# Optimization experiments

Measured on AMD Instinct MI355X. Metric: run time of the kernel, lower is better.

## Reference

```python
import math
import jax, jax.numpy as jnp
import numpy as np

H = 512        # d_model
NST = 32       # N // 2 complex states
M = 2          # frac_M
CH = 1         # channels
L_DEFAULT = 2048
OMIN, OMAX = 1e-06, 100.0
EMIN, EMAX = 1e-06, 10.0


def _logit_init(vals, vmin, vmax):
    v = np.clip(np.asarray(vals, np.float32), vmin, vmax)
    p = np.clip((v - vmin) / (vmax - vmin), 1e-06, 1.0 - 1e-06)
    return np.log(p / (1.0 - p)).astype(np.float32)


def setup_inputs() -> dict:
    key = jax.random.key(0)
    k1, k2 = jax.random.split(key, 2)
    # log_dt ~ U[log(dt_min), log(dt_max)]
    log_dt = (jax.random.uniform(k1, (H,), dtype=jnp.float32)
              * (math.log(0.1) - math.log(0.001)) + math.log(0.001))
    # C stored as real view of complex [CH, H, NST]
    C_real = jax.random.normal(k2, (CH, H, NST, 2), dtype=jnp.float32)
    log_A_real = jnp.log(0.5 * jnp.ones((H, NST), jnp.float32))
    A_imag = math.pi * jnp.broadcast_to(jnp.arange(NST, dtype=jnp.float32), (H, NST))
    # frac_M == 2 defaults: omega=[0.0, 0.1], eta=[1.0, 0.1], stored as logits
    omega_logit = jnp.asarray(_logit_init([0.0, 0.1], OMIN, OMAX))
    eta_logit = jnp.asarray(_logit_init([1.0, 0.1], EMIN, EMAX))
    return {"C_real": C_real, "log_dt": log_dt, "log_A_real": log_A_real,
            "A_imag": A_imag, "omega_logit": omega_logit,
            "eta_logit": eta_logit, "L": L_DEFAULT}


def reference(C_real, log_dt, log_A_real, A_imag, omega_logit, eta_logit, L):
    dt = jnp.exp(log_dt)                                   # [H]
    C = C_real[..., 0] + 1j * C_real[..., 1]               # [CH, H, NST] complex
    A = -jnp.exp(log_A_real) + 1j * A_imag                 # [H, NST] complex
    omega = OMIN + jax.nn.sigmoid(omega_logit) * (OMAX - OMIN)  # [M]
    eta = EMIN + jax.nn.sigmoid(eta_logit) * (EMAX - EMIN)      # [M]
    # fractional mixture of poles: A_frac[h, m, n] = -omega_m + eta_m * A[h, n]
    A_frac = (-omega[None, :, None] + eta[None, :, None] * A[:, None, :]).reshape(H, M * NST)
    C_frac = (eta[None, None, :, None] * C[:, :, None, :]).reshape(CH, H, M * NST)
    dtA = A_frac * dt[:, None]                             # [H, M*NST]
    exp_dtA = jnp.exp(dtA)
    small = jnp.abs(A_frac) < 1e-06
    C_disc = C_frac * (exp_dtA[None] - 1.0) / (A_frac[None] + 1e-08)
    C_disc = jnp.where(small[None], C_frac * dt[None, :, None], C_disc)
    t = jnp.arange(L, dtype=jnp.float32)
    exp_K = jnp.exp(dtA[:, :, None] * t)                   # [H, M*NST, L] complex Vandermonde
    K = 2.0 * jnp.einsum('chn,hnl->chl', C_disc, exp_K).real  # [CH, H, L]
    return K
```

## Files before the change

kernel.cpp:

```cpp
#include <hip/hip_runtime.h>
#include <math.h>

#define HH   512
#define NST  32
#define MM   2
#define LL   2048
#define NS   (MM * NST)
#define TL   8

__global__ __launch_bounds__(256) void loong_kernel(
    const float* __restrict__ C_real,
    const float* __restrict__ log_dt,
    const float* __restrict__ log_A_real,
    const float* __restrict__ A_imag,
    const float* __restrict__ omega_logit,
    const float* __restrict__ eta_logit,
    float* __restrict__ out)
{
    __shared__ float4 sT1[NS][16];
    __shared__ float4 sT2[NS][16];

    const int h   = blockIdx.x;
    const int tid = threadIdx.x;

    if (tid < NS) {
        const int m = tid >> 5;
        const int n = tid & 31;
        const float dt  = expf(log_dt[h]);
        const float Are = -expf(log_A_real[h * NST + n]);
        const float Aim = A_imag[h * NST + n];
        const float om = 1e-6f + (100.0f - 1e-6f) / (1.0f + expf(-omega_logit[m]));
        const float et = 1e-6f + (10.0f  - 1e-6f) / (1.0f + expf(-eta_logit[m]));
        const float Afr = fmaf(et, Are, -om);
        const float Afi = et * Aim;
        const float Cfr = et * C_real[(h * NST + n) * 2 + 0];
        const float Cfi = et * C_real[(h * NST + n) * 2 + 1];
        const float ar = dt * Afr, ai = dt * Afi;
        const float e = expf(ar);
        float sn, cs;
        sincosf(ai, &sn, &cs);
        const float Er = e * cs, Ei = e * sn;
        const float dr = Afr + 1e-8f, di = Afi;
        const float inv = 1.0f / fmaf(dr, dr, di * di);
        const float numr = Er - 1.0f, numi = Ei;
        const float fr = fmaf(numr, dr,  numi * di) * inv;
        const float fi = fmaf(numi, dr, -numr * di) * inv;
        float Cdr = fmaf(Cfr, fr, -(Cfi * fi));
        float Cdi = fmaf(Cfr, fi,  (Cfi * fr));
        if (sqrtf(fmaf(Afr, Afr, Afi * Afi)) < 1e-6f) {
            Cdr = Cfr * dt;
            Cdi = Cfi * dt;
        }
        const float Ccr = 2.0f * Cdr, Cci = 2.0f * Cdi;
        const float p  = 2.0f * Er;
        const float qc = -fmaf(Er, Er, Ei * Ei);

        float w2r = fmaf(Er, Er, -(Ei * Ei)),  w2i = 2.0f * Er * Ei;
        float w4r = fmaf(w2r, w2r, -(w2i * w2i)), w4i = 2.0f * w2r * w2i;
        float w8r = fmaf(w4r, w4r, -(w4i * w4i)), w8i = 2.0f * w4r * w4i;

        float ur = 1.0f, ui = 0.0f;
#pragma unroll
        for (int r = 0; r < 16; ++r) {
            sT1[tid][r] = make_float4(ur, ui,
                                      fmaf(ur, Er, -(ui * Ei)),
                                      fmaf(ur, Ei,  (ui * Er)));
            const float nr = fmaf(ur, w8r, -(ui * w8i));
            const float ni = fmaf(ur, w8i,  (ui * w8r));
            ur = nr; ui = ni;
        }
        float wr_ = w8r, wi_ = w8i;
#pragma unroll
        for (int k = 0; k < 4; ++k) {
            const float nr = fmaf(wr_, wr_, -(wi_ * wi_));
            const float ni = 2.0f * wr_ * wi_;
            wr_ = nr; wi_ = ni;
        }
        float vr = Ccr, vi = Cci;
#pragma unroll
        for (int q = 0; q < 16; ++q) {
            sT2[tid][q] = make_float4(vr, vi, p, qc);
            const float nr = fmaf(vr, wr_, -(vi * wi_));
            const float ni = fmaf(vr, wi_,  (vi * wr_));
            vr = nr; vi = ni;
        }
    }
    __syncthreads();

    const int ri = tid & 15;
    const int qi = tid >> 4;

    float acc[TL];
#pragma unroll
    for (int j = 0; j < TL; ++j) acc[j] = 0.0f;

    for (int s = 0; s < NS; s += 4) {
        float4 t1[4], t2[4];
#pragma unroll
        for (int u = 0; u < 4; ++u) {
            t1[u] = sT1[s + u][ri];
            t2[u] = sT2[s + u][qi];
        }
#pragma unroll
        for (int u = 0; u < 4; ++u) {
            const float p = t2[u].z, qq = t2[u].w;
            float r0 = fmaf(t1[u].x, t2[u].x, -(t1[u].y * t2[u].y));
            float r1 = fmaf(t1[u].z, t2[u].x, -(t1[u].w * t2[u].y));
            acc[0] += r0;
            acc[1] += r1;
#pragma unroll
            for (int j = 2; j < TL; ++j) {
                const float rn = fmaf(p, r1, qq * r0);
                acc[j] += rn;
                r0 = r1; r1 = rn;
            }
        }
    }

    float4* o = reinterpret_cast<float4*>(out + (size_t)h * LL + (size_t)tid * TL);
    o[0] = make_float4(acc[0], acc[1], acc[2], acc[3]);
    o[1] = make_float4(acc[4], acc[5], acc[6], acc[7]);
}

extern "C" void kernel_launch(void* const* d_in, const int* in_sizes, int n_in,
                              void* d_out, int out_size, void* d_ws, size_t ws_size,
                              hipStream_t stream) {
    const float* C_real      = (const float*)d_in[0];
    const float* log_dt      = (const float*)d_in[1];
    const float* log_A_real  = (const float*)d_in[2];
    const float* A_imag      = (const float*)d_in[3];
    const float* omega_logit = (const float*)d_in[4];
    const float* eta_logit   = (const float*)d_in[5];
    float* out = (float*)d_out;

    loong_kernel<<<dim3(HH), dim3(256), 0, stream>>>(
        C_real, log_dt, log_A_real, A_imag, omega_logit, eta_logit, out);
}
```

Measured before the change: 74.92 us.

## Spread table setup over all threads, swizzle LDS tables, double-buffer LDS loads

Table setup now runs on all 256 threads: each of the 64 states is split into four parts, and each part writes 8 of the 16 T1 or T2 entries, seeded with w^64 or w^1024 jumps. Before, only 64 threads built the tables serially. The LDS tables are XOR-swizzled by state index to spread the accesses across shared-memory banks. The main loop is double-buffered so LDS reads for the next group of states are issued while the current group is computed. The trade is more redundant pole and exp computation per thread, and more registers for the two load buffers.

```diff
diff --git a/kernel.cpp b/kernel.cpp
--- a/kernel.cpp
+++ b/kernel.cpp
@@ -23,9 +23,11 @@
     const int h   = blockIdx.x;
     const int tid = threadIdx.x;
 
-    if (tid < NS) {
-        const int m = tid >> 5;
-        const int n = tid & 31;
+    {
+        const int s    = tid & (NS - 1);
+        const int part = tid >> 6;
+        const int m = s >> 5;
+        const int n = s & 31;
         const float dt  = expf(log_dt[h]);
         const float Are = -expf(log_A_real[h * NST + n]);
         const float Aim = A_imag[h * NST + n];
@@ -55,34 +57,47 @@
         const float p  = 2.0f * Er;
         const float qc = -fmaf(Er, Er, Ei * Ei);
 
-        float w2r = fmaf(Er, Er, -(Ei * Ei)),  w2i = 2.0f * Er * Ei;
-        float w4r = fmaf(w2r, w2r, -(w2i * w2i)), w4i = 2.0f * w2r * w2i;
-        float w8r = fmaf(w4r, w4r, -(w4i * w4i)), w8i = 2.0f * w4r * w4i;
+        const float w2r = fmaf(Er, Er, -(Ei * Ei)),     w2i = 2.0f * Er * Ei;
+        const float w4r = fmaf(w2r, w2r, -(w2i * w2i)), w4i = 2.0f * w2r * w2i;
+        const float w8r = fmaf(w4r, w4r, -(w4i * w4i)), w8i = 2.0f * w4r * w4i;
+        const float w16r  = fmaf(w8r,  w8r,  -(w8i  * w8i)),  w16i  = 2.0f * w8r  * w8i;
+        const float w32r  = fmaf(w16r, w16r, -(w16i * w16i)), w32i  = 2.0f * w16r * w16i;
+        const float w64r  = fmaf(w32r, w32r, -(w32i * w32i)), w64i  = 2.0f * w32r * w32i;
+        const float w128r = fmaf(w64r, w64r, -(w64i * w64i)), w128i = 2.0f * w64r * w64i;
+        const float w256r  = fmaf(w128r, w128r, -(w128i * w128i)), w256i  = 2.0f * w128r * w128i;
+        const float w512r  = fmaf(w256r, w256r, -(w256i * w256i)), w512i  = 2.0f * w256r * w256i;
+        const float w1024r = fmaf(w512r, w512r, -(w512i * w512i)), w1024i = 2.0f * w512r * w512i;
 
-        float ur = 1.0f, ui = 0.0f;
+        if (part < 2) {
+            float ur = 1.0f, ui = 0.0f;
+            if (part == 1) { ur = w64r; ui = w64i; }
+            const int base = part << 3;
 #pragma unroll
-        for (int r = 0; r < 16; ++r) {
-            sT1[tid][r] = make_float4(ur, ui,
-                                      fmaf(ur, Er, -(ui * Ei)),
-                                      fmaf(ur, Ei,  (ui * Er)));
-            const float nr = fmaf(ur, w8r, -(ui * w8i));
-            const float ni = fmaf(ur, w8i,  (ui * w8r));
-            ur = nr; ui = ni;
-        }
-        float wr_ = w8r, wi_ = w8i;
+            for (int r = 0; r < 8; ++r) {
+                const int e = base + r;
+                sT1[s][e ^ (s & 15)] = make_float4(ur, ui,
+                                                   fmaf(ur, Er, -(ui * Ei)),
+                                                   fmaf(ur, Ei,  (ui * Er)));
+                const float nr = fmaf(ur, w8r, -(ui * w8i));
+                const float ni = fmaf(ur, w8i,  (ui * w8r));
+                ur = nr; ui = ni;
+            }
+        } else {
+            float vr = Ccr, vi = Cci;
+            if (part == 3) {
+                const float tr = fmaf(vr, w1024r, -(vi * w1024i));
+                const float ti = fmaf(vr, w1024i,  (vi * w1024r));
+                vr = tr; vi = ti;
+            }
+            const int base = (part & 1) << 3;
 #pragma unroll
-        for (int k = 0; k < 4; ++k) {
-            const float nr = fmaf(wr_, wr_, -(wi_ * wi_));
-            const float ni = 2.0f * wr_ * wi_;
-            wr_ = nr; wi_ = ni;
-        }
-        float vr = Ccr, vi = Cci;
-#pragma unroll
-        for (int q = 0; q < 16; ++q) {
-            sT2[tid][q] = make_float4(vr, vi, p, qc);
-            const float nr = fmaf(vr, wr_, -(vi * wi_));
-            const float ni = fmaf(vr, wi_,  (vi * wr_));
-            vr = nr; vi = ni;
+            for (int q = 0; q < 8; ++q) {
+                const int e = base + q;
+                sT2[s][e ^ (s & 15)] = make_float4(vr, vi, p, qc);
+                const float nr = fmaf(vr, w128r, -(vi * w128i));
+                const float ni = fmaf(vr, w128i,  (vi * w128r));
+                vr = nr; vi = ni;
+            }
         }
     }
     __syncthreads();
@@ -94,28 +109,46 @@
 #pragma unroll
     for (int j = 0; j < TL; ++j) acc[j] = 0.0f;
 
-    for (int s = 0; s < NS; s += 4) {
-        float4 t1[4], t2[4];
+    float4 A1[4], A2[4], B1[4], B2[4];
+
+#define LOADG(T1v, T2v, S0)                                            \
+    _Pragma("unroll")                                                  \
+    for (int u = 0; u < 4; ++u) {                                      \
+        const int ss = (S0) + u;                                       \
+        T1v[u] = sT1[ss][ri ^ (ss & 15)];                              \
+        T2v[u] = sT2[ss][qi ^ (ss & 15)];                              \
+    }
+
+#define COMPG(T1v, T2v)                                                \
+    _Pragma("unroll")                                                  \
+    for (int u = 0; u < 4; ++u) {                                      \
+        const float pp = T2v[u].z, qq = T2v[u].w;                      \
+        float r0 = fmaf(T1v[u].x, T2v[u].x, -(T1v[u].y * T2v[u].y));   \
+        float r1 = fmaf(T1v[u].z, T2v[u].x, -(T1v[u].w * T2v[u].y));   \
+        acc[0] += r0;                                                  \
+        acc[1] += r1;                                                  \
+        _Pragma("unroll")                                              \
+        for (int j = 2; j < TL; ++j) {                                 \
+            const float rn = fmaf(pp, r1, qq * r0);                    \
+            acc[j] += rn;                                              \
+            r0 = r1; r1 = rn;                                          \
+        }                                                              \
+    }
+
+    LOADG(A1, A2, 0)
 #pragma unroll
-        for (int u = 0; u < 4; ++u) {
-            t1[u] = sT1[s + u][ri];
-            t2[u] = sT2[s + u][qi];
-        }
-#pragma unroll
-        for (int u = 0; u < 4; ++u) {
-            const float p = t2[u].z, qq = t2[u].w;
-            float r0 = fmaf(t1[u].x, t2[u].x, -(t1[u].y * t2[u].y));
-            float r1 = fmaf(t1[u].z, t2[u].x, -(t1[u].w * t2[u].y));
-            acc[0] += r0;
-            acc[1] += r1;
-#pragma unroll
-            for (int j = 2; j < TL; ++j) {
-                const float rn = fmaf(p, r1, qq * r0);
-                acc[j] += rn;
-                r0 = r1; r1 = rn;
-            }
-        }
+    for (int g = 0; g < 7; ++g) {
+        LOADG(B1, B2, 8 * g + 4)
+        COMPG(A1, A2)
+        LOADG(A1, A2, 8 * g + 8)
+        COMPG(B1, B2)
     }
+    LOADG(B1, B2, 60)
+    COMPG(A1, A2)
+    COMPG(B1, B2)
+
+#undef LOADG
+#undef COMPG
 
     float4* o = reinterpret_cast<float4*>(out + (size_t)h * LL + (size_t)tid * TL);
     o[0] = make_float4(acc[0], acc[1], acc[2], acc[3]);
```

Measured after the change: 73.31 us. 2.1% less time.

## Split states across waves with 32-step recurrences and shared-memory reduction

Applied to the files above, without the earlier changes.

Each wave now takes 16 of the 64 states. Each thread runs a 32-step second-order recurrence per state, so a thread covers 32 output positions instead of 8. The per-wave partial sums then go through a swizzled shared-memory buffer and are added across the four waves. All 256 threads now build the power table in parallel, where before only 64 threads did. The aim is to cut table-build serialization and shared-memory reads per output. The cost is a larger accumulator array per thread (register pressure), an extra reduction pass with two more barriers, and longer recurrences that may lose float accuracy.

```diff
diff --git a/kernel.cpp b/kernel.cpp
--- a/kernel.cpp
+++ b/kernel.cpp
@@ -6,9 +6,9 @@
 #define MM   2
 #define LL   2048
 #define NS   (MM * NST)
-#define TL   8
+#define NT   256
 
-__global__ __launch_bounds__(256) void loong_kernel(
+__global__ __launch_bounds__(NT) void loong_kernel(
     const float* __restrict__ C_real,
     const float* __restrict__ log_dt,
     const float* __restrict__ log_A_real,
@@ -17,15 +17,21 @@
     const float* __restrict__ eta_logit,
     float* __restrict__ out)
 {
-    __shared__ float4 sT1[NS][16];
-    __shared__ float4 sT2[NS][16];
+    __shared__ __align__(16) float sbuf[64 * 64 * 2 + 64 * 4];
+    float2* T1z = reinterpret_cast<float2*>(sbuf);
+    float4* U   = reinterpret_cast<float4*>(sbuf + 8192);
+    float4* sR  = reinterpret_cast<float4*>(sbuf);
 
     const int h   = blockIdx.x;
     const int tid = threadIdx.x;
+    const int wv  = tid >> 6;
+    const int ln  = tid & 63;
 
-    if (tid < NS) {
-        const int m = tid >> 5;
-        const int n = tid & 31;
+    {
+        const int s    = ln;
+        const int part = wv;
+        const int m = s >> 5;
+        const int n = s & 31;
         const float dt  = expf(log_dt[h]);
         const float Are = -expf(log_A_real[h * NST + n]);
         const float Aim = A_imag[h * NST + n];
@@ -52,74 +58,121 @@
             Cdi = Cfi * dt;
         }
         const float Ccr = 2.0f * Cdr, Cci = 2.0f * Cdi;
-        const float p  = 2.0f * Er;
-        const float qc = -fmaf(Er, Er, Ei * Ei);
 
-        float w2r = fmaf(Er, Er, -(Ei * Ei)),  w2i = 2.0f * Er * Ei;
-        float w4r = fmaf(w2r, w2r, -(w2i * w2i)), w4i = 2.0f * w2r * w2i;
-        float w8r = fmaf(w4r, w4r, -(w4i * w4i)), w8i = 2.0f * w4r * w4i;
-
-        float ur = 1.0f, ui = 0.0f;
+        float xr = Er, xi = Ei;
 #pragma unroll
-        for (int r = 0; r < 16; ++r) {
-            sT1[tid][r] = make_float4(ur, ui,
-                                      fmaf(ur, Er, -(ui * Ei)),
-                                      fmaf(ur, Ei,  (ui * Er)));
-            const float nr = fmaf(ur, w8r, -(ui * w8i));
-            const float ni = fmaf(ur, w8i,  (ui * w8r));
-            ur = nr; ui = ni;
+        for (int k = 0; k < 5; ++k) {
+            const float nr = fmaf(xr, xr, -(xi * xi));
+            const float ni = 2.0f * xr * xi;
+            xr = nr; xi = ni;
         }
-        float wr_ = w8r, wi_ = w8i;
+        const float w32r = xr, w32i = xi;
+        float yr = w32r, yi = w32i;
 #pragma unroll
         for (int k = 0; k < 4; ++k) {
-            const float nr = fmaf(wr_, wr_, -(wi_ * wi_));
-            const float ni = 2.0f * wr_ * wi_;
-            wr_ = nr; wi_ = ni;
+            const float nr = fmaf(yr, yr, -(yi * yi));
+            const float ni = 2.0f * yr * yi;
+            yr = nr; yi = ni;
         }
-        float vr = Ccr, vi = Cci;
+        const float t16r = yr, t16i = yi;
+        const float t32r = fmaf(t16r, t16r, -(t16i * t16i));
+        const float t32i = 2.0f * t16r * t16i;
+        const float t48r = fmaf(t32r, t16r, -(t32i * t16i));
+        const float t48i = fmaf(t32r, t16i,  (t32i * t16r));
+
+        float cr = 1.0f, ci = 0.0f;
+        if      (part == 1) { cr = t16r; ci = t16i; }
+        else if (part == 2) { cr = t32r; ci = t32i; }
+        else if (part == 3) { cr = t48r; ci = t48i; }
+
 #pragma unroll
-        for (int q = 0; q < 16; ++q) {
-            sT2[tid][q] = make_float4(vr, vi, p, qc);
-            const float nr = fmaf(vr, wr_, -(vi * wi_));
-            const float ni = fmaf(vr, wi_,  (vi * wr_));
-            vr = nr; vi = ni;
+        for (int k = 0; k < 16; ++k) {
+            const int col = (16 * part + k) ^ s;
+            T1z[s * 64 + col] = make_float2(cr, ci);
+            const float nr = fmaf(cr, w32r, -(ci * w32i));
+            const float ni = fmaf(cr, w32i,  (ci * w32r));
+            cr = nr; ci = ni;
+        }
+        if (part == 0) U[s] = make_float4(Ccr, Cci, Er, Ei);
+    }
+    __syncthreads();
+
+    float acc[32];
+#pragma unroll
+    for (int j = 0; j < 32; ++j) acc[j] = 0.0f;
+
+    const int sb = wv << 4;
+
+#define STATE_COMP(u, Uv)                                              \
+    {                                                                  \
+        const float zr = fmaf((u).x, (Uv).x, -((u).y * (Uv).y));       \
+        const float zi = fmaf((u).x, (Uv).y,  ((u).y * (Uv).x));       \
+        const float wr = (Uv).z, wi = (Uv).w;                          \
+        const float p  = wr + wr;                                      \
+        const float qn = fmaf(wr, wr, wi * wi);                        \
+        float r0 = zr;                                                 \
+        float r1 = fmaf(zr, wr, -(zi * wi));                           \
+        acc[0] += r0;                                                  \
+        acc[1] += r1;                                                  \
+        _Pragma("unroll")                                              \
+        for (int j = 2; j < 32; ++j) {                                 \
+            const float t  = qn * r0;                                  \
+            const float rn = fmaf(p, r1, -t);                          \
+            acc[j] += rn;                                              \
+            r0 = r1; r1 = rn;                                          \
+        }                                                              \
+    }
+
+    float2 uA = T1z[(sb + 0) * 64 + (ln ^ (sb + 0))];
+    float4 UA = U[sb + 0];
+    float2 uB = T1z[(sb + 1) * 64 + (ln ^ (sb + 1))];
+    float4 UB = U[sb + 1];
+#pragma unroll
+    for (int i = 0; i < 8; ++i) {
+        float2 nuA = uA, nuB = uB;
+        float4 nUA = UA, nUB = UB;
+        if (i < 7) {
+            const int sA = sb + 2 * i + 2, sBt = sA + 1;
+            nuA = T1z[sA * 64 + (ln ^ sA)];
+            nUA = U[sA];
+            nuB = T1z[sBt * 64 + (ln ^ sBt)];
+            nUB = U[sBt];
+        }
+        STATE_COMP(uA, UA)
+        STATE_COMP(uB, UB)
+        uA = nuA; UA = nUA; uB = nuB; UB = nUB;
+    }
+#undef STATE_COMP
+
+    __syncthreads();
+    {
+        float4* sRw = sR + wv * 512;
+#pragma unroll
+        for (int c = 0; c < 8; ++c) {
+            const int scol = 8 * ln + (c ^ (ln & 7));
+            sRw[scol] = make_float4(acc[4 * c + 0], acc[4 * c + 1],
+                                    acc[4 * c + 2], acc[4 * c + 3]);
         }
     }
     __syncthreads();
-
-    const int ri = tid & 15;
-    const int qi = tid >> 4;
-
-    float acc[TL];
+    {
+        float4* op = reinterpret_cast<float4*>(out + (size_t)h * LL);
 #pragma unroll
-    for (int j = 0; j < TL; ++j) acc[j] = 0.0f;
-
-    for (int s = 0; s < NS; s += 4) {
-        float4 t1[4], t2[4];
-#pragma unroll
-        for (int u = 0; u < 4; ++u) {
-            t1[u] = sT1[s + u][ri];
-            t2[u] = sT2[s + u][qi];
-        }
-#pragma unroll
-        for (int u = 0; u < 4; ++u) {
-            const float p = t2[u].z, qq = t2[u].w;
-            float r0 = fmaf(t1[u].x, t2[u].x, -(t1[u].y * t2[u].y));
-            float r1 = fmaf(t1[u].z, t2[u].x, -(t1[u].w * t2[u].y));
-            acc[0] += r0;
-            acc[1] += r1;
-#pragma unroll
-            for (int j = 2; j < TL; ++j) {
-                const float rn = fmaf(p, r1, qq * r0);
-                acc[j] += rn;
-                r0 = r1; r1 = rn;
-            }
+        for (int k = 0; k < 2; ++k) {
+            const int col  = (wv << 7) + (k << 6) + ln;
+            const int scol = (col & ~7) | ((col & 7) ^ ((col >> 3) & 7));
+            const float4 a = sR[scol];
+            const float4 b = sR[512 + scol];
+            const float4 c4 = sR[1024 + scol];
+            const float4 d = sR[1536 + scol];
+            float4 sm;
+            sm.x = (a.x + b.x) + (c4.x + d.x);
+            sm.y = (a.y + b.y) + (c4.y + d.y);
+            sm.z = (a.z + b.z) + (c4.z + d.z);
+            sm.w = (a.w + b.w) + (c4.w + d.w);
+            op[col] = sm;
         }
     }
-
-    float4* o = reinterpret_cast<float4*>(out + (size_t)h * LL + (size_t)tid * TL);
-    o[0] = make_float4(acc[0], acc[1], acc[2], acc[3]);
-    o[1] = make_float4(acc[4], acc[5], acc[6], acc[7]);
 }
 
 extern "C" void kernel_launch(void* const* d_in, const int* in_sizes, int n_in,
@@ -133,6 +186,6 @@
     const float* eta_logit   = (const float*)d_in[5];
     float* out = (float*)d_out;
 
-    loong_kernel<<<dim3(HH), dim3(256), 0, stream>>>(
+    loong_kernel<<<dim3(HH), dim3(NT), 0, stream>>>(
         C_real, log_dt, log_A_real, A_imag, omega_logit, eta_logit, out);
 }
```

New measurement: 72.98 us. 2.6% less time.
